# Kernel tuning notes

Measured on AMD Instinct MI355X. Metric: run time of the kernel, lower is better.

## Reference

```python
import jax, jax.numpy as jnp
import numpy as np

BLOCK = 8

def _dct_matrix(N: int) -> jnp.ndarray:
    # DCT-II orthonormal matrix, matches the torch double loop
    k = np.arange(N)[:, None]
    n = np.arange(N)[None, :]
    mat = np.sqrt(2.0 / N) * np.cos(np.pi * k * (2 * n + 1) / (2 * N))
    mat[0, :] = np.sqrt(1.0 / N)
    return jnp.asarray(mat, dtype=jnp.float32)

def _haar_dwt(x):
    x00 = x[:, :, 0::2, 0::2]
    x01 = x[:, :, 0::2, 1::2]
    x10 = x[:, :, 1::2, 0::2]
    x11 = x[:, :, 1::2, 1::2]
    LL = (x00 + x01 + x10 + x11) * 0.5
    LH = (x00 + x01 - x10 - x11) * 0.5
    HL = (x00 - x01 + x10 - x11) * 0.5
    HH = (x00 - x01 - x10 + x11) * 0.5
    return LL, LH, HL, HH

def _block_dct2(x, D):
    # x: [B,C,H,W] -> blockwise 2D DCT with BLOCK x BLOCK tiles
    B, C, H, W = x.shape
    bs = BLOCK
    blocks = x.reshape(B, C, H // bs, bs, W // bs, bs)
    blocks = blocks.transpose(0, 1, 2, 4, 3, 5)  # [B,C,Hb,Wb,bs,bs]
    out = jnp.einsum('km,bchwmn,ln->bchwkl', D, blocks, D)  # D @ X @ D^T
    out = out.transpose(0, 1, 2, 4, 3, 5).reshape(B, C, H, W)
    return out

def setup_inputs() -> dict:
    key = jax.random.key(0)
    x = jax.random.normal(key, (16, 3, 1024, 1024), dtype=jnp.float32)
    return {"x": x}

def reference(x):
    D = _dct_matrix(BLOCK)
    LL, LH, HL, HH = _haar_dwt(x)
    LL_dct = _block_dct2(LL, D)
    return (LL_dct, LH, HL, HH)
```

## Files before the change

kernel.cpp:

```cpp
#include <hip/hip_runtime.h>
#include <math.h>


#define NOUT ((size_t)48 * 512 * 512)

#define C0 0.35355339059327376f
#define C1 0.49039264020161522f
#define C2 0.46193976625564337f
#define C3 0.41573480615127262f
#define C4 0.35355339059327376f
#define C5 0.27778511650980111f
#define C6 0.19134171618254489f
#define C7 0.09754516100806414f

#define LD4(dst, src) do { float4 _v = *(const float4*)(src); \
    (dst)[0]=_v.x; (dst)[1]=_v.y; (dst)[2]=_v.z; (dst)[3]=_v.w; } while(0)

__global__ __launch_bounds__(256) void hfe_kernel(const float* __restrict__ x,
                                                  float* __restrict__ out) {
    static constexpr float DMc[8][8] = {
        { C0,  C0,  C0,  C0,  C0,  C0,  C0,  C0},
        { C1,  C3,  C5,  C7, -C7, -C5, -C3, -C1},
        { C2,  C6, -C6, -C2, -C2, -C6,  C6,  C2},
        { C3, -C7, -C1, -C5,  C5,  C1,  C7, -C3},
        { C4, -C4, -C4,  C4,  C4, -C4, -C4,  C4},
        { C5, -C1,  C7,  C3, -C3, -C7,  C1, -C5},
        { C6, -C2,  C2, -C6, -C6,  C2, -C2,  C6},
        { C7, -C5,  C3, -C1,  C1, -C3,  C5, -C7},
    };

    __shared__ float4 T4[16][33];
    __shared__ float  Dm[8][8];

    const int t = threadIdx.x;

    if (t < 64) {
        const int k = t >> 3, n = t & 7;
        double v = (k == 0) ? 0.35355339059327376220
                            : 0.5 * cos(M_PI * (double)(k * (2 * n + 1)) / 16.0);
        Dm[k][n] = (float)v;
    }

    const int bid = blockIdx.x;
    const int bc  = bid >> 7;
    const int rem = bid & 127;
    const int ty  = rem >> 2;
    const int tx  = rem & 3;

    const size_t img_in  = (size_t)bc * (1024 * 1024);
    const size_t img_out = (size_t)bc * (512 * 512);

    const int hr   = t >> 4;
    const int bcol = t & 15;

    const int in_row = ty * 32 + hr * 2;
    const int in_col = tx * 256 + bcol * 16;
    const float* p0 = x + img_in + (size_t)in_row * 1024 + in_col;
    const float* p1 = p0 + 1024;

    float e[16], o[16];
    LD4(&e[0], p0 + 0); LD4(&e[4], p0 + 4); LD4(&e[8], p0 + 8); LD4(&e[12], p0 + 12);
    LD4(&o[0], p1 + 0); LD4(&o[4], p1 + 4); LD4(&o[8], p1 + 8); LD4(&o[12], p1 + 12);

    float ll[8], lh[8], hl[8], hh[8];
#pragma unroll
    for (int n = 0; n < 8; ++n) {
        const float s1 = e[2*n] + e[2*n+1], d1 = e[2*n] - e[2*n+1];
        const float s2 = o[2*n] + o[2*n+1], d2 = o[2*n] - o[2*n+1];
        ll[n] = (s1 + s2) * 0.5f;
        lh[n] = (s1 - s2) * 0.5f;
        hl[n] = (d1 + d2) * 0.5f;
        hh[n] = (d1 - d2) * 0.5f;
    }

    const int h_row = ty * 16 + hr;
    const int h_col = tx * 128 + bcol * 8;
    float* ob = out + img_out + (size_t)h_row * 512 + h_col;
    *(float4*)(ob + NOUT)         = make_float4(lh[0], lh[1], lh[2], lh[3]);
    *(float4*)(ob + NOUT + 4)     = make_float4(lh[4], lh[5], lh[6], lh[7]);
    *(float4*)(ob + 2 * NOUT)     = make_float4(hl[0], hl[1], hl[2], hl[3]);
    *(float4*)(ob + 2 * NOUT + 4) = make_float4(hl[4], hl[5], hl[6], hl[7]);
    *(float4*)(ob + 3 * NOUT)     = make_float4(hh[0], hh[1], hh[2], hh[3]);
    *(float4*)(ob + 3 * NOUT + 4) = make_float4(hh[4], hh[5], hh[6], hh[7]);

    float tr[8];
#pragma unroll
    for (int l = 0; l < 8; ++l) {
        float acc = ll[0] * DMc[l][0];
#pragma unroll
        for (int n = 1; n < 8; ++n) acc = fmaf(ll[n], DMc[l][n], acc);
        tr[l] = acc;
    }
    T4[hr][bcol * 2]     = make_float4(tr[0], tr[1], tr[2], tr[3]);
    T4[hr][bcol * 2 + 1] = make_float4(tr[4], tr[5], tr[6], tr[7]);

    __syncthreads();

    const int orow = t >> 4;
    const int bc2  = t & 15;
    const int brow = orow >> 3;
    const int k    = orow & 7;

    float Dk[8];
#pragma unroll
    for (int m = 0; m < 8; ++m) Dk[m] = Dm[k][m];

    float4 a0 = make_float4(0.f, 0.f, 0.f, 0.f);
    float4 a1 = a0;
#pragma unroll
    for (int m = 0; m < 8; ++m) {
        const float dk = Dk[m];
        const float4 t0 = T4[brow * 8 + m][bc2 * 2];
        const float4 t1 = T4[brow * 8 + m][bc2 * 2 + 1];
        a0.x = fmaf(dk, t0.x, a0.x); a0.y = fmaf(dk, t0.y, a0.y);
        a0.z = fmaf(dk, t0.z, a0.z); a0.w = fmaf(dk, t0.w, a0.w);
        a1.x = fmaf(dk, t1.x, a1.x); a1.y = fmaf(dk, t1.y, a1.y);
        a1.z = fmaf(dk, t1.z, a1.z); a1.w = fmaf(dk, t1.w, a1.w);
    }

    float* oc = out + img_out + (size_t)(ty * 16 + orow) * 512 + tx * 128 + bc2 * 8;
    *(float4*)(oc)     = a0;
    *(float4*)(oc + 4) = a1;
}

extern "C" void kernel_launch(void* const* d_in, const int* in_sizes, int n_in,
                              void* d_out, int out_size, void* d_ws, size_t ws_size,
                              hipStream_t stream) {
    const float* x = (const float*)d_in[0];
    float* out = (float*)d_out;
    hfe_kernel<<<dim3(6144), dim3(256), 0, stream>>>(x, out);
}
```

Before: 331.3 us.

## Shrink tiles to 8x64 half-res per block with nontemporal stores and staged DCT

Restructures the kernel so each block covers an 8-row by 64-column half-resolution tile (four times more blocks), each thread loading one float4 from each of two input rows and producing two outputs per subband. The row DCT is moved to 64 threads working from a shared-memory LL tile, followed by a column DCT done by all threads. Subband and DCT outputs use nontemporal 2-wide stores, and the DCT table comes from a constant array instead of being computed with double-precision cos. The goal is better memory parallelism and coalescing and less per-thread work. In exchange it adds an extra barrier, leaves most threads idle during the row-DCT stage, and uses narrower stores.

```diff
diff --git a/kernel.cpp b/kernel.cpp
--- a/kernel.cpp
+++ b/kernel.cpp
@@ -1,6 +1,7 @@
 #include <hip/hip_runtime.h>
-#include <math.h>
 
+
+typedef float f32x2 __attribute__((ext_vector_type(2)));
 
 #define NOUT ((size_t)48 * 512 * 512)
 
@@ -13,8 +14,16 @@
 #define C6 0.19134171618254489f
 #define C7 0.09754516100806414f
 
-#define LD4(dst, src) do { float4 _v = *(const float4*)(src); \
-    (dst)[0]=_v.x; (dst)[1]=_v.y; (dst)[2]=_v.z; (dst)[3]=_v.w; } while(0)
+__device__ __constant__ float DCT_TAB[64] = {
+     C0,  C0,  C0,  C0,  C0,  C0,  C0,  C0,
+     C1,  C3,  C5,  C7, -C7, -C5, -C3, -C1,
+     C2,  C6, -C6, -C2, -C2, -C6,  C6,  C2,
+     C3, -C7, -C1, -C5,  C5,  C1,  C7, -C3,
+     C4, -C4, -C4,  C4,  C4, -C4, -C4,  C4,
+     C5, -C1,  C7,  C3, -C3, -C7,  C1, -C5,
+     C6, -C2,  C2, -C6, -C6,  C2, -C2,  C6,
+     C7, -C5,  C3, -C1,  C1, -C3,  C5, -C7,
+};
 
 __global__ __launch_bounds__(256) void hfe_kernel(const float* __restrict__ x,
                                                   float* __restrict__ out) {
@@ -29,98 +38,81 @@
         { C7, -C5,  C3, -C1,  C1, -C3,  C5, -C7},
     };
 
-    __shared__ float4 T4[16][33];
-    __shared__ float  Dm[8][8];
+    __shared__ float M[8][68];
+    __shared__ float U[8][68];
+    __shared__ float Dm[8][8];
 
     const int t = threadIdx.x;
-
-    if (t < 64) {
-        const int k = t >> 3, n = t & 7;
-        double v = (k == 0) ? 0.35355339059327376220
-                            : 0.5 * cos(M_PI * (double)(k * (2 * n + 1)) / 16.0);
-        Dm[k][n] = (float)v;
-    }
+    if (t < 64) Dm[t >> 3][t & 7] = DCT_TAB[t];
 
     const int bid = blockIdx.x;
-    const int bc  = bid >> 7;
-    const int rem = bid & 127;
-    const int ty  = rem >> 2;
-    const int tx  = rem & 3;
+    const int bc  = bid >> 9;
+    const int rem = bid & 511;
+    const int ty  = rem >> 3;
+    const int tx  = rem & 7;
 
     const size_t img_in  = (size_t)bc * (1024 * 1024);
     const size_t img_out = (size_t)bc * (512 * 512);
 
-    const int hr   = t >> 4;
-    const int bcol = t & 15;
+    const int hr = t >> 5;
+    const int cp = t & 31;
 
-    const int in_row = ty * 32 + hr * 2;
-    const int in_col = tx * 256 + bcol * 16;
-    const float* p0 = x + img_in + (size_t)in_row * 1024 + in_col;
-    const float* p1 = p0 + 1024;
+    const float* p0 = x + img_in + (size_t)(ty * 16 + hr * 2) * 1024 + tx * 128 + cp * 4;
+    const float4 a = *(const float4*)(p0);
+    const float4 b = *(const float4*)(p0 + 1024);
 
-    float e[16], o[16];
-    LD4(&e[0], p0 + 0); LD4(&e[4], p0 + 4); LD4(&e[8], p0 + 8); LD4(&e[12], p0 + 12);
-    LD4(&o[0], p1 + 0); LD4(&o[4], p1 + 4); LD4(&o[8], p1 + 8); LD4(&o[12], p1 + 12);
+    const float s1 = a.x + a.y, d1 = a.x - a.y;
+    const float s2 = b.x + b.y, d2 = b.x - b.y;
+    const float s3 = a.z + a.w, d3 = a.z - a.w;
+    const float s4 = b.z + b.w, d4 = b.z - b.w;
 
-    float ll[8], lh[8], hl[8], hh[8];
-#pragma unroll
-    for (int n = 0; n < 8; ++n) {
-        const float s1 = e[2*n] + e[2*n+1], d1 = e[2*n] - e[2*n+1];
-        const float s2 = o[2*n] + o[2*n+1], d2 = o[2*n] - o[2*n+1];
-        ll[n] = (s1 + s2) * 0.5f;
-        lh[n] = (s1 - s2) * 0.5f;
-        hl[n] = (d1 + d2) * 0.5f;
-        hh[n] = (d1 - d2) * 0.5f;
-    }
+    const float ll0 = (s1 + s2) * 0.5f, lh0 = (s1 - s2) * 0.5f;
+    const float hl0 = (d1 + d2) * 0.5f, hh0 = (d1 - d2) * 0.5f;
+    const float ll1 = (s3 + s4) * 0.5f, lh1 = (s3 - s4) * 0.5f;
+    const float hl1 = (d3 + d4) * 0.5f, hh1 = (d3 - d4) * 0.5f;
 
-    const int h_row = ty * 16 + hr;
-    const int h_col = tx * 128 + bcol * 8;
-    float* ob = out + img_out + (size_t)h_row * 512 + h_col;
-    *(float4*)(ob + NOUT)         = make_float4(lh[0], lh[1], lh[2], lh[3]);
-    *(float4*)(ob + NOUT + 4)     = make_float4(lh[4], lh[5], lh[6], lh[7]);
-    *(float4*)(ob + 2 * NOUT)     = make_float4(hl[0], hl[1], hl[2], hl[3]);
-    *(float4*)(ob + 2 * NOUT + 4) = make_float4(hl[4], hl[5], hl[6], hl[7]);
-    *(float4*)(ob + 3 * NOUT)     = make_float4(hh[0], hh[1], hh[2], hh[3]);
-    *(float4*)(ob + 3 * NOUT + 4) = make_float4(hh[4], hh[5], hh[6], hh[7]);
+    const size_t hidx = img_out + (size_t)(ty * 8 + hr) * 512 + tx * 64 + cp * 2;
+    __builtin_nontemporal_store((f32x2){lh0, lh1}, (f32x2*)(out + NOUT     + hidx));
+    __builtin_nontemporal_store((f32x2){hl0, hl1}, (f32x2*)(out + 2 * NOUT + hidx));
+    __builtin_nontemporal_store((f32x2){hh0, hh1}, (f32x2*)(out + 3 * NOUT + hidx));
 
-    float tr[8];
-#pragma unroll
-    for (int l = 0; l < 8; ++l) {
-        float acc = ll[0] * DMc[l][0];
-#pragma unroll
-        for (int n = 1; n < 8; ++n) acc = fmaf(ll[n], DMc[l][n], acc);
-        tr[l] = acc;
-    }
-    T4[hr][bcol * 2]     = make_float4(tr[0], tr[1], tr[2], tr[3]);
-    T4[hr][bcol * 2 + 1] = make_float4(tr[4], tr[5], tr[6], tr[7]);
+    *(f32x2*)&M[hr][cp * 2] = (f32x2){ll0, ll1};
 
     __syncthreads();
 
-    const int orow = t >> 4;
-    const int bc2  = t & 15;
-    const int brow = orow >> 3;
-    const int k    = orow & 7;
+    if (t < 64) {
+        const int b8 = (t >> 3) * 8;
+        const int r  = t & 7;
+        float m[8];
+        *(float4*)&m[0] = *(const float4*)&M[r][b8];
+        *(float4*)&m[4] = *(const float4*)&M[r][b8 + 4];
+        float u[8];
+#pragma unroll
+        for (int l = 0; l < 8; ++l) {
+            float acc = m[0] * DMc[l][0];
+#pragma unroll
+            for (int n = 1; n < 8; ++n) acc = fmaf(m[n], DMc[l][n], acc);
+            u[l] = acc;
+        }
+        *(float4*)&U[r][b8]     = *(float4*)&u[0];
+        *(float4*)&U[r][b8 + 4] = *(float4*)&u[4];
+    }
 
+    __syncthreads();
+
+    const int k = t >> 5;
     float Dk[8];
 #pragma unroll
     for (int m = 0; m < 8; ++m) Dk[m] = Dm[k][m];
 
-    float4 a0 = make_float4(0.f, 0.f, 0.f, 0.f);
-    float4 a1 = a0;
+    float o0 = 0.f, o1 = 0.f;
 #pragma unroll
     for (int m = 0; m < 8; ++m) {
-        const float dk = Dk[m];
-        const float4 t0 = T4[brow * 8 + m][bc2 * 2];
-        const float4 t1 = T4[brow * 8 + m][bc2 * 2 + 1];
-        a0.x = fmaf(dk, t0.x, a0.x); a0.y = fmaf(dk, t0.y, a0.y);
-        a0.z = fmaf(dk, t0.z, a0.z); a0.w = fmaf(dk, t0.w, a0.w);
-        a1.x = fmaf(dk, t1.x, a1.x); a1.y = fmaf(dk, t1.y, a1.y);
-        a1.z = fmaf(dk, t1.z, a1.z); a1.w = fmaf(dk, t1.w, a1.w);
+        const f32x2 um = *(const f32x2*)&U[m][cp * 2];
+        o0 = fmaf(Dk[m], um.x, o0);
+        o1 = fmaf(Dk[m], um.y, o1);
     }
-
-    float* oc = out + img_out + (size_t)(ty * 16 + orow) * 512 + tx * 128 + bc2 * 8;
-    *(float4*)(oc)     = a0;
-    *(float4*)(oc + 4) = a1;
+    __builtin_nontemporal_store((f32x2){o0, o1}, (f32x2*)(out + hidx));
 }
 
 extern "C" void kernel_launch(void* const* d_in, const int* in_sizes, int n_in,
@@ -128,5 +120,5 @@
                               hipStream_t stream) {
     const float* x = (const float*)d_in[0];
     float* out = (float*)d_out;
-    hfe_kernel<<<dim3(6144), dim3(256), 0, stream>>>(x, out);
+    hfe_kernel<<<dim3(24576), dim3(256), 0, stream>>>(x, out);
 }
```

Measured after the change: 334.0 us. No clear change (+0.8%).
